# Kernel optimization log

Hardware: AMD Instinct MI355X
Metric: run time of the kernel (lower is better)

The kernel has to match this reference:

```python
import jax, jax.numpy as jnp
import numpy as np

B, T, V, D, H, O = 64, 256, 50000, 512, 1024, 64


def setup_inputs() -> dict:
    key = jax.random.key(0)
    ks = jax.random.split(key, 8)
    s = 1.0 / np.sqrt(H)  # PyTorch GRU/Linear init range
    x = jax.random.randint(ks[0], (B, T), 0, V)
    emb = jax.random.normal(ks[1], (V, D), dtype=jnp.float32) * 0.02
    W_ih = jax.random.uniform(ks[2], (3 * H, D), jnp.float32, -s, s)
    W_hh = jax.random.uniform(ks[3], (3 * H, H), jnp.float32, -s, s)
    b_ih = jax.random.uniform(ks[4], (3 * H,), jnp.float32, -s, s)
    b_hh = jax.random.uniform(ks[5], (3 * H,), jnp.float32, -s, s)
    W_fc = jax.random.uniform(ks[6], (O, H), jnp.float32, -s, s)
    b_fc = jax.random.uniform(ks[7], (O,), jnp.float32, -s, s)
    return {"x": x, "emb": emb, "W_ih": W_ih, "W_hh": W_hh,
            "b_ih": b_ih, "b_hh": b_hh, "W_fc": W_fc, "b_fc": b_fc}


def _gru_seq(gates_x, W_hh, b_hh, h0):
    # gates_x: [T, B, 3H] precomputed input contributions (r|z|n order, as PyTorch)
    def step(h, gx):
        gh = h @ W_hh.T + b_hh                       # [B, 3H]
        xr, xz, xn = jnp.split(gx, 3, axis=-1)
        hr, hz, hn = jnpp_split(gh) if False else jnp.split(gh, 3, axis=-1)
        r = jax.nn.sigmoid(xr + hr)
        z = jax.nn.sigmoid(xz + hz)
        n = jnp.tanh(xn + r * hn)
        h_new = (1.0 - z) * n + z * h
        return h_new, h_new

    _, hs = jax.lax.scan(step, h0, gates_x)          # hs: [T, B, H]
    return hs


def reference(x, emb, W_ih, W_hh, b_ih, b_hh, W_fc, b_fc):
    xe = emb[x]                                      # [B, T, D]
    # Precompute all input-to-gate projections in one GEMM: [B, T, 3H]
    gates_x = jnp.einsum('btd,gd->btg', xe, W_ih) + b_ih
    h0 = jnp.zeros((x.shape[0], W_hh.shape[1]), dtype=xe.dtype)
    hs = _gru_seq(jnp.swapaxes(gates_x, 0, 1), W_hh, b_hh, h0)  # [T, B, H]
    out = jnp.swapaxes(hs, 0, 1)                     # [B, T, H]
    logits = jnp.einsum('bth,oh->bto', out, W_fc) + b_fc
    proba = jax.nn.sigmoid(logits)
    predicted_labels = (proba > 0.5).astype(jnp.float32)
    return proba, predicted_labels
```

## Files before the change

### kernel.cpp

```cpp
#include <hip/hip_runtime.h>
#include <math.h>

#define B_   64
#define T_   256
#define D_   512
#define H_   1024
#define G3_  3072
#define O_   64
#define NTOK (B_*T_)
#define TC_  64
#define NCH_ 4

__global__ __launch_bounds__(256) void init_ws(double* __restrict__ hs,
                                               int* __restrict__ flags)
{
  int idx = blockIdx.x*256 + threadIdx.x;
  hs[idx] = 0.0;
  if (idx < 4096) flags[idx] = 0;
}

__global__ __launch_bounds__(256) void stage_a(
    const int* __restrict__ x, const float* __restrict__ emb,
    const float* __restrict__ W_ih, const float* __restrict__ b_ih,
    double* __restrict__ gx, int t_base)
{
  __shared__ float As[64][33];
  __shared__ float Bs[64][33];
  const int tid = threadIdx.x;
  const int b = blockIdx.x & 63, nBlk = blockIdx.x >> 6;
  const int g0 = nBlk*64;

  const int r = tid >> 2, c8 = tid & 3;
  const float* ap = emb  + (size_t)x[b*T_ + t_base + r]*D_ + c8*8;
  const float* bp = W_ih + (size_t)(g0 + r)*D_ + c8*8;
  const int tx = tid & 15, ty = tid >> 4;

  double acc[4][4];
  #pragma unroll
  for (int i = 0; i < 4; ++i)
    #pragma unroll
    for (int j = 0; j < 4; ++j) acc[i][j] = 0.0;

  float4 a0 = *(const float4*)(ap), a1 = *(const float4*)(ap + 4);
  float4 b0 = *(const float4*)(bp), b1 = *(const float4*)(bp + 4);

  for (int kb = 0; kb < 16; ++kb){
    __syncthreads();
    As[r][c8*8+0]=a0.x; As[r][c8*8+1]=a0.y; As[r][c8*8+2]=a0.z; As[r][c8*8+3]=a0.w;
    As[r][c8*8+4]=a1.x; As[r][c8*8+5]=a1.y; As[r][c8*8+6]=a1.z; As[r][c8*8+7]=a1.w;
    Bs[r][c8*8+0]=b0.x; Bs[r][c8*8+1]=b0.y; Bs[r][c8*8+2]=b0.z; Bs[r][c8*8+3]=b0.w;
    Bs[r][c8*8+4]=b1.x; Bs[r][c8*8+5]=b1.y; Bs[r][c8*8+6]=b1.z; Bs[r][c8*8+7]=b1.w;
    __syncthreads();
    if (kb < 15){
      a0 = *(const float4*)(ap + (kb+1)*32);  a1 = *(const float4*)(ap + (kb+1)*32 + 4);
      b0 = *(const float4*)(bp + (kb+1)*32);  b1 = *(const float4*)(bp + (kb+1)*32 + 4);
    }
    #pragma unroll
    for (int k = 0; k < 32; ++k){
      double av[4], bv[4];
      #pragma unroll
      for (int i = 0; i < 4; ++i) av[i] = (double)As[ty*4+i][k];
      #pragma unroll
      for (int j = 0; j < 4; ++j) bv[j] = (double)Bs[tx*4+j][k];
      #pragma unroll
      for (int i = 0; i < 4; ++i)
        #pragma unroll
        for (int j = 0; j < 4; ++j) acc[i][j] = fma(av[i], bv[j], acc[i][j]);
    }
  }

  double bi[4];
  #pragma unroll
  for (int j = 0; j < 4; ++j) bi[j] = (double)b_ih[g0 + tx*4 + j];
  #pragma unroll
  for (int i = 0; i < 4; ++i){
    int tl = ty*4 + i;
    size_t rowoff = ((size_t)tl*B_ + b)*G3_ + g0 + tx*4;
    #pragma unroll
    for (int j = 0; j < 4; ++j)
      gx[rowoff + j] = acc[i][j] + bi[j];
  }
}

__global__ __launch_bounds__(256, 1) void gru_rec(
    const float* __restrict__ W_hh, const float* __restrict__ b_hh,
    const double* __restrict__ gx, double* __restrict__ hs,
    int* __restrict__ flags, int t_base)
{
  __shared__ double Wl[2*12*514];
  __shared__ int abort_flag;
  const int tid = threadIdx.x, wg = blockIdx.x;
  const int i0 = wg*4;
  if (tid == 0) abort_flag = 0;

  for (int it = tid; it < 12*1024; it += 256){
    int rr = it >> 10, k = it & 1023;
    int p = rr >> 2, j = rr & 3;
    int hf = k >> 9, kl = k & 511;
    Wl[(hf*12 + rr)*514 + kl] = (double)W_hh[(size_t)(p*H_ + i0 + j)*H_ + k];
  }

  const int bq = tid >> 3, j = (tid >> 1) & 3, half = tid & 1;
  const int b_out = bq*2 + half;
  const int jj = i0 + j;
  const double bh0 = (double)b_hh[jj];
  const double bh1 = (double)b_hh[H_   + jj];
  const double bh2 = (double)b_hh[2*H_ + jj];
  const double2* w0p = (const double2*)&Wl[(half*12 + 0*4 + j)*514];
  const double2* w1p = (const double2*)&Wl[(half*12 + 1*4 + j)*514];
  const double2* w2p = (const double2*)&Wl[(half*12 + 2*4 + j)*514];
  __syncthreads();

  double hprev = hs[(size_t)b_out*H_ + jj];

  for (int tt = 0; tt < TC_; ++tt){
    const int t = t_base + tt;

    const double* gp = gx + ((size_t)tt*B_ + b_out)*G3_ + jj;
    double gxr = gp[0];
    double gxz = gp[H_];
    double gxn = gp[2*H_];

    {
      int* fp = flags + tid*16;
      int gcnt = 0;
      while (__hip_atomic_load(fp, __ATOMIC_RELAXED, __HIP_MEMORY_SCOPE_AGENT) < t){
        __builtin_amdgcn_s_sleep(2);
        if (++gcnt > (1<<18)) { abort_flag = 1; break; }
      }
    }
    __syncthreads();
    if (abort_flag) break;

    const double2* h0 = (const double2*)(hs + ((size_t)tt*B_ + bq*2    )*H_ + half*512);
    const double2* h1 = (const double2*)(hs + ((size_t)tt*B_ + bq*2 + 1)*H_ + half*512);

    double pr00=0.0, pr10=0.0, pr20=0.0, pr01=0.0, pr11=0.0, pr21=0.0;
    #pragma unroll 8
    for (int kk = 0; kk < 256; ++kk){
      double2 a0 = h0[kk];
      double2 a1 = h1[kk];
      double2 w0 = w0p[kk];
      double2 w1 = w1p[kk];
      double2 w2 = w2p[kk];
      pr00 = fma(a0.x, w0.x, pr00); pr00 = fma(a0.y, w0.y, pr00);
      pr10 = fma(a0.x, w1.x, pr10); pr10 = fma(a0.y, w1.y, pr10);
      pr20 = fma(a0.x, w2.x, pr20); pr20 = fma(a0.y, w2.y, pr20);
      pr01 = fma(a1.x, w0.x, pr01); pr01 = fma(a1.y, w0.y, pr01);
      pr11 = fma(a1.x, w1.x, pr11); pr11 = fma(a1.y, w1.y, pr11);
      pr21 = fma(a1.x, w2.x, pr21); pr21 = fma(a1.y, w2.y, pr21);
    }
    double s00 = pr00 + __shfl_xor(pr00, 1);
    double s01 = pr01 + __shfl_xor(pr01, 1);
    double s10 = pr10 + __shfl_xor(pr10, 1);
    double s11 = pr11 + __shfl_xor(pr11, 1);
    double s20 = pr20 + __shfl_xor(pr20, 1);
    double s21 = pr21 + __shfl_xor(pr21, 1);
    double ar = half ? s01 : s00;
    double az = half ? s11 : s10;
    double an = half ? s21 : s20;

    double rr_ = 1.0/(1.0 + exp(-(gxr + ar + bh0)));
    double zz  = 1.0/(1.0 + exp(-(gxz + az + bh1)));
    double nn  = tanh(gxn + rr_*(an + bh2));
    double hnew = (1.0 - zz)*nn + zz*hprev;
    hprev = hnew;

    __hip_atomic_store(&hs[((size_t)(tt+1)*B_ + b_out)*H_ + jj], hnew,
                       __ATOMIC_RELAXED, __HIP_MEMORY_SCOPE_AGENT);
    if (tt == TC_-1)
      __hip_atomic_store(&hs[(size_t)b_out*H_ + jj], hnew,
                         __ATOMIC_RELAXED, __HIP_MEMORY_SCOPE_AGENT);

    asm volatile("s_waitcnt vmcnt(0)" ::: "memory");
    __syncthreads();
    if (tid == 0)
      __hip_atomic_store(flags + wg*16, t+1, __ATOMIC_RELAXED, __HIP_MEMORY_SCOPE_AGENT);
  }
}

__global__ __launch_bounds__(256) void fc_out(
    const double* __restrict__ hs, const float* __restrict__ W_fc,
    const float* __restrict__ b_fc, float* __restrict__ out, int t_base)
{
  __shared__ double Ah[64][34];
  __shared__ double Bw[64][34];
  const int tid = threadIdx.x;
  const int b = blockIdx.x;
  const int r = tid >> 2, c8 = tid & 3;
  const double* ap = hs   + ((size_t)(r+1)*B_ + b)*H_ + c8*8;
  const float*  bp = W_fc + (size_t)r*H_ + c8*8;
  const int tx = tid & 15, ty = tid >> 4;

  double acc[4][4];
  #pragma unroll
  for (int i = 0; i < 4; ++i)
    #pragma unroll
    for (int j = 0; j < 4; ++j) acc[i][j] = 0.0;

  double ar0[8]; float br0[8];
  #pragma unroll
  for (int e = 0; e < 8; ++e){ ar0[e] = ap[e]; br0[e] = bp[e]; }

  for (int kb = 0; kb < 32; ++kb){
    __syncthreads();
    #pragma unroll
    for (int e = 0; e < 8; ++e){
      Ah[r][c8*8+e] = ar0[e];
      Bw[r][c8*8+e] = (double)br0[e];
    }
    __syncthreads();
    if (kb < 31){
      #pragma unroll
      for (int e = 0; e < 8; ++e){
        ar0[e] = ap[(kb+1)*32 + e];
        br0[e] = bp[(kb+1)*32 + e];
      }
    }
    #pragma unroll
    for (int k = 0; k < 32; ++k){
      double av[4], bv[4];
      #pragma unroll
      for (int i = 0; i < 4; ++i) av[i] = Ah[ty*4+i][k];
      #pragma unroll
      for (int j = 0; j < 4; ++j) bv[j] = Bw[tx*4+j][k];
      #pragma unroll
      for (int i = 0; i < 4; ++i)
        #pragma unroll
        for (int j = 0; j < 4; ++j) acc[i][j] = fma(av[i], bv[j], acc[i][j]);
    }
  }

  double bi[4];
  #pragma unroll
  for (int j = 0; j < 4; ++j) bi[j] = (double)b_fc[tx*4 + j];
  #pragma unroll
  for (int i = 0; i < 4; ++i){
    int tl = ty*4 + i;
    size_t tok = (size_t)b*T_ + t_base + tl;
    float4 pr, lb;
    float* prp = (float*)&pr; float* lbp = (float*)&lb;
    #pragma unroll
    for (int j = 0; j < 4; ++j){
      double logit = acc[i][j] + bi[j];
      prp[j] = (float)(1.0/(1.0 + exp(-logit)));
      float lf = (float)logit;
      float ef = (float)exp(-(double)lf);
      float pf = 1.0f / (1.0f + ef);
      lbp[j] = (pf > 0.5f) ? 1.0f : 0.0f;
    }
    *(float4*)&out[tok*O_ + tx*4] = pr;
    *(float4*)&out[(size_t)NTOK*O_ + tok*O_ + tx*4] = lb;
  }
}

extern "C" void kernel_launch(void* const* d_in, const int* in_sizes, int n_in,
                              void* d_out, int out_size, void* d_ws, size_t ws_size,
                              hipStream_t stream) {
  const int*   x    = (const int*)  d_in[0];
  const float* emb  = (const float*)d_in[1];
  const float* W_ih = (const float*)d_in[2];
  const float* W_hh = (const float*)d_in[3];
  const float* b_ih = (const float*)d_in[4];
  const float* b_hh = (const float*)d_in[5];
  const float* W_fc = (const float*)d_in[6];
  const float* b_fc = (const float*)d_in[7];
  float* out = (float*)d_out;
  char* ws = (char*)d_ws;

  double* gx    = (double*)(ws);
  double* hs    = (double*)(ws + 100663296);
  int*    flags = (int*)   (ws + 134742016);

  hipLaunchKernelGGL(init_ws, dim3(256), dim3(256), 0, stream, hs, flags);
  for (int c = 0; c < NCH_; ++c){
    int t_base = c*TC_;
    hipLaunchKernelGGL(stage_a, dim3(3072), dim3(256), 0, stream,
                       x, emb, W_ih, b_ih, gx, t_base);
    hipLaunchKernelGGL(gru_rec, dim3(256), dim3(256), 0, stream,
                       W_hh, b_hh, gx, hs, flags, t_base);
    hipLaunchKernelGGL(fc_out, dim3(64), dim3(256), 0, stream,
                       hs, W_fc, b_fc, out, t_base);
  }
}
```

Measured before the change: 9.848 ms.

## Split GRU recurrence K-dimension across 8 lanes with 512-thread blocks

The persistent GRU recurrence kernel now runs 512 threads per block. Each thread handles a 128-wide slice of the hidden dimension for 4 batch rows, instead of a 512-wide slice for 2 rows, and partial sums are combined with a three-level butterfly shuffle. This shortens the serial dot-product chain per timestep and gives each loaded weight more reuse across batch rows. The cost is redundant loads of gate inputs, more shuffles and more register pressure, and only half the threads store results.

New measurement: 17.12 ms. +73.8%, slower.

```diff
diff --git a/kernel.cpp b/kernel.cpp
--- a/kernel.cpp
+++ b/kernel.cpp
@@ -82,33 +82,37 @@
   }
 }
 
-__global__ __launch_bounds__(256, 1) void gru_rec(
+__global__ __launch_bounds__(512, 1) void gru_rec(
     const float* __restrict__ W_hh, const float* __restrict__ b_hh,
     const double* __restrict__ gx, double* __restrict__ hs,
     int* __restrict__ flags, int t_base)
 {
-  __shared__ double Wl[2*12*514];
+  __shared__ double Wl[96*130];
   __shared__ int abort_flag;
   const int tid = threadIdx.x, wg = blockIdx.x;
   const int i0 = wg*4;
   if (tid == 0) abort_flag = 0;
 
-  for (int it = tid; it < 12*1024; it += 256){
-    int rr = it >> 10, k = it & 1023;
+  for (int idx = tid; idx < 12*1024; idx += 512){
+    int rr = idx >> 10, k = idx & 1023;
     int p = rr >> 2, j = rr & 3;
-    int hf = k >> 9, kl = k & 511;
-    Wl[(hf*12 + rr)*514 + kl] = (double)W_hh[(size_t)(p*H_ + i0 + j)*H_ + k];
-  }
-
-  const int bq = tid >> 3, j = (tid >> 1) & 3, half = tid & 1;
-  const int b_out = bq*2 + half;
+    int ksl = k >> 7, kl = k & 127;
+    Wl[(rr*8 + ksl)*130 + kl] = (double)W_hh[(size_t)(p*H_ + i0 + j)*H_ + k];
+  }
+
+  const int ks = tid & 7;
+  const int j  = (tid >> 3) & 3;
+  const int bg = tid >> 5;
+  const int b0 = bg*4;
+  const int b_out = b0 + (ks & 3);
+  const bool owner = (ks < 4);
   const int jj = i0 + j;
   const double bh0 = (double)b_hh[jj];
   const double bh1 = (double)b_hh[H_   + jj];
   const double bh2 = (double)b_hh[2*H_ + jj];
-  const double2* w0p = (const double2*)&Wl[(half*12 + 0*4 + j)*514];
-  const double2* w1p = (const double2*)&Wl[(half*12 + 1*4 + j)*514];
-  const double2* w2p = (const double2*)&Wl[(half*12 + 2*4 + j)*514];
+  const double2* w0p = (const double2*)&Wl[((0*4 + j)*8 + ks)*130];
+  const double2* w1p = (const double2*)&Wl[((1*4 + j)*8 + ks)*130];
+  const double2* w2p = (const double2*)&Wl[((2*4 + j)*8 + ks)*130];
   __syncthreads();
 
   double hprev = hs[(size_t)b_out*H_ + jj];
@@ -121,7 +125,7 @@
     double gxz = gp[H_];
     double gxn = gp[2*H_];
 
-    {
+    if (tid < 256){
       int* fp = flags + tid*16;
       int gcnt = 0;
       while (__hip_atomic_load(fp, __ATOMIC_RELAXED, __HIP_MEMORY_SCOPE_AGENT) < t){
@@ -132,45 +136,64 @@
     __syncthreads();
     if (abort_flag) break;
 
-    const double2* h0 = (const double2*)(hs + ((size_t)tt*B_ + bq*2    )*H_ + half*512);
-    const double2* h1 = (const double2*)(hs + ((size_t)tt*B_ + bq*2 + 1)*H_ + half*512);
-
-    double pr00=0.0, pr10=0.0, pr20=0.0, pr01=0.0, pr11=0.0, pr21=0.0;
-    #pragma unroll 8
-    for (int kk = 0; kk < 256; ++kk){
-      double2 a0 = h0[kk];
-      double2 a1 = h1[kk];
+    const double2* h0p = (const double2*)(hs + ((size_t)tt*B_ + b0+0)*H_ + ks*128);
+    const double2* h1p = (const double2*)(hs + ((size_t)tt*B_ + b0+1)*H_ + ks*128);
+    const double2* h2p = (const double2*)(hs + ((size_t)tt*B_ + b0+2)*H_ + ks*128);
+    const double2* h3p = (const double2*)(hs + ((size_t)tt*B_ + b0+3)*H_ + ks*128);
+
+    double pr[3][4];
+    #pragma unroll
+    for (int g = 0; g < 3; ++g)
+      #pragma unroll
+      for (int i = 0; i < 4; ++i) pr[g][i] = 0.0;
+
+    #pragma unroll 4
+    for (int kk = 0; kk < 64; ++kk){
+      double2 a[4];
+      a[0] = h0p[kk]; a[1] = h1p[kk]; a[2] = h2p[kk]; a[3] = h3p[kk];
       double2 w0 = w0p[kk];
       double2 w1 = w1p[kk];
       double2 w2 = w2p[kk];
-      pr00 = fma(a0.x, w0.x, pr00); pr00 = fma(a0.y, w0.y, pr00);
-      pr10 = fma(a0.x, w1.x, pr10); pr10 = fma(a0.y, w1.y, pr10);
-      pr20 = fma(a0.x, w2.x, pr20); pr20 = fma(a0.y, w2.y, pr20);
-      pr01 = fma(a1.x, w0.x, pr01); pr01 = fma(a1.y, w0.y, pr01);
-      pr11 = fma(a1.x, w1.x, pr11); pr11 = fma(a1.y, w1.y, pr11);
-      pr21 = fma(a1.x, w2.x, pr21); pr21 = fma(a1.y, w2.y, pr21);
-    }
-    double s00 = pr00 + __shfl_xor(pr00, 1);
-    double s01 = pr01 + __shfl_xor(pr01, 1);
-    double s10 = pr10 + __shfl_xor(pr10, 1);
-    double s11 = pr11 + __shfl_xor(pr11, 1);
-    double s20 = pr20 + __shfl_xor(pr20, 1);
-    double s21 = pr21 + __shfl_xor(pr21, 1);
-    double ar = half ? s01 : s00;
-    double az = half ? s11 : s10;
-    double an = half ? s21 : s20;
-
-    double rr_ = 1.0/(1.0 + exp(-(gxr + ar + bh0)));
-    double zz  = 1.0/(1.0 + exp(-(gxz + az + bh1)));
-    double nn  = tanh(gxn + rr_*(an + bh2));
+      #pragma unroll
+      for (int i = 0; i < 4; ++i){
+        pr[0][i] = fma(a[i].x, w0.x, pr[0][i]); pr[0][i] = fma(a[i].y, w0.y, pr[0][i]);
+        pr[1][i] = fma(a[i].x, w1.x, pr[1][i]); pr[1][i] = fma(a[i].y, w1.y, pr[1][i]);
+        pr[2][i] = fma(a[i].x, w2.x, pr[2][i]); pr[2][i] = fma(a[i].y, w2.y, pr[2][i]);
+      }
+    }
+
+    #pragma unroll
+    for (int g = 0; g < 3; ++g)
+      #pragma unroll
+      for (int i = 0; i < 4; ++i){
+        double v = pr[g][i];
+        v += __shfl_xor(v, 1);
+        v += __shfl_xor(v, 2);
+        v += __shfl_xor(v, 4);
+        pr[g][i] = v;
+      }
+
+    double sg[3];
+    #pragma unroll
+    for (int g = 0; g < 3; ++g){
+      double sA = (ks & 1) ? pr[g][1] : pr[g][0];
+      double sB = (ks & 1) ? pr[g][3] : pr[g][2];
+      sg[g] = (ks & 2) ? sB : sA;
+    }
+
+    double rr_ = 1.0/(1.0 + exp(-(gxr + sg[0] + bh0)));
+    double zz  = 1.0/(1.0 + exp(-(gxz + sg[1] + bh1)));
+    double nn  = tanh(gxn + rr_*(sg[2] + bh2));
     double hnew = (1.0 - zz)*nn + zz*hprev;
     hprev = hnew;
 
-    __hip_atomic_store(&hs[((size_t)(tt+1)*B_ + b_out)*H_ + jj], hnew,
-                       __ATOMIC_RELAXED, __HIP_MEMORY_SCOPE_AGENT);
-    if (tt == TC_-1)
-      __hip_atomic_store(&hs[(size_t)b_out*H_ + jj], hnew,
+    if (owner){
+      __hip_atomic_store(&hs[((size_t)(tt+1)*B_ + b_out)*H_ + jj], hnew,
                          __ATOMIC_RELAXED, __HIP_MEMORY_SCOPE_AGENT);
+      if (tt == TC_-1)
+        __hip_atomic_store(&hs[(size_t)b_out*H_ + jj], hnew,
+                           __ATOMIC_RELAXED, __HIP_MEMORY_SCOPE_AGENT);
+    }
 
     asm volatile("s_waitcnt vmcnt(0)" ::: "memory");
     __syncthreads();
@@ -277,7 +300,7 @@
     int t_base = c*TC_;
     hipLaunchKernelGGL(stage_a, dim3(3072), dim3(256), 0, stream,
                        x, emb, W_ih, b_ih, gx, t_base);
-    hipLaunchKernelGGL(gru_rec, dim3(256), dim3(256), 0, stream,
+    hipLaunchKernelGGL(gru_rec, dim3(256), dim3(512), 0, stream,
                        W_hh, b_hh, gx, hs, flags, t_base);
     hipLaunchKernelGGL(fc_out, dim3(64), dim3(256), 0, stream,
                        hs, W_fc, b_fc, out, t_base);
```

## Register-tile GRU recurrence over 4 batches x 4 columns with shuffle-tree reduction

Applied to the files above, without the earlier changes.

Replaces the LDS-staged fp64 copy of the W_hh slice with float4 reads straight from global memory (which should stay in cache across timesteps). Each thread now computes a 4-batch by 4-column by 3-gate register tile over a 64-element slice of k, instead of 2 batches by 3 gates over half of k. The 16 k-partials are combined with a butterfly of xor shuffles that halves the live values at each level. This raises reuse of h and W per load and drops the LDS weight traffic. In exchange it carries 48 fp64 accumulators per thread (register pressure) and depends on cache hits for the weights every step.

Result: slower. 15.45 ms (+56.9%).

```diff
diff --git a/kernel.cpp b/kernel.cpp
--- a/kernel.cpp
+++ b/kernel.cpp
@@ -87,36 +87,36 @@
     const double* __restrict__ gx, double* __restrict__ hs,
     int* __restrict__ flags, int t_base)
 {
-  __shared__ double Wl[2*12*514];
   __shared__ int abort_flag;
   const int tid = threadIdx.x, wg = blockIdx.x;
   const int i0 = wg*4;
   if (tid == 0) abort_flag = 0;
 
-  for (int it = tid; it < 12*1024; it += 256){
-    int rr = it >> 10, k = it & 1023;
-    int p = rr >> 2, j = rr & 3;
-    int hf = k >> 9, kl = k & 511;
-    Wl[(hf*12 + rr)*514 + kl] = (double)W_hh[(size_t)(p*H_ + i0 + j)*H_ + k];
-  }
-
-  const int bq = tid >> 3, j = (tid >> 1) & 3, half = tid & 1;
-  const int b_out = bq*2 + half;
-  const int jj = i0 + j;
-  const double bh0 = (double)b_hh[jj];
-  const double bh1 = (double)b_hh[H_   + jj];
-  const double bh2 = (double)b_hh[2*H_ + jj];
-  const double2* w0p = (const double2*)&Wl[(half*12 + 0*4 + j)*514];
-  const double2* w1p = (const double2*)&Wl[(half*12 + 1*4 + j)*514];
-  const double2* w2p = (const double2*)&Wl[(half*12 + 2*4 + j)*514];
+  const int bq4 = tid >> 4, k16 = tid & 15;
+  const int B0  = bq4*4;
+  const int cb1 = (k16 >> 3) & 1, cb0 = (k16 >> 2) & 1;
+  const int bb1 = (k16 >> 1) & 1, bb0 = k16 & 1;
+  const int b_out = B0 + (k16 & 3);
+  const int c_out = i0 + (k16 >> 2);
+
+  const double bh0 = (double)b_hh[c_out];
+  const double bh1 = (double)b_hh[H_   + c_out];
+  const double bh2 = (double)b_hh[2*H_ + c_out];
+
+  const float4* wp[3][4];
+  #pragma unroll
+  for (int p = 0; p < 3; ++p)
+    #pragma unroll
+    for (int c = 0; c < 4; ++c)
+      wp[p][c] = (const float4*)(W_hh + (size_t)(p*H_ + i0 + c)*H_ + k16*64);
+
+  double hprev = hs[(size_t)b_out*H_ + c_out];
   __syncthreads();
-
-  double hprev = hs[(size_t)b_out*H_ + jj];
 
   for (int tt = 0; tt < TC_; ++tt){
     const int t = t_base + tt;
 
-    const double* gp = gx + ((size_t)tt*B_ + b_out)*G3_ + jj;
+    const double* gp = gx + ((size_t)tt*B_ + b_out)*G3_ + c_out;
     double gxr = gp[0];
     double gxz = gp[H_];
     double gxn = gp[2*H_];
@@ -132,44 +132,111 @@
     __syncthreads();
     if (abort_flag) break;
 
-    const double2* h0 = (const double2*)(hs + ((size_t)tt*B_ + bq*2    )*H_ + half*512);
-    const double2* h1 = (const double2*)(hs + ((size_t)tt*B_ + bq*2 + 1)*H_ + half*512);
-
-    double pr00=0.0, pr10=0.0, pr20=0.0, pr01=0.0, pr11=0.0, pr21=0.0;
-    #pragma unroll 8
-    for (int kk = 0; kk < 256; ++kk){
-      double2 a0 = h0[kk];
-      double2 a1 = h1[kk];
-      double2 w0 = w0p[kk];
-      double2 w1 = w1p[kk];
-      double2 w2 = w2p[kk];
-      pr00 = fma(a0.x, w0.x, pr00); pr00 = fma(a0.y, w0.y, pr00);
-      pr10 = fma(a0.x, w1.x, pr10); pr10 = fma(a0.y, w1.y, pr10);
-      pr20 = fma(a0.x, w2.x, pr20); pr20 = fma(a0.y, w2.y, pr20);
-      pr01 = fma(a1.x, w0.x, pr01); pr01 = fma(a1.y, w0.y, pr01);
-      pr11 = fma(a1.x, w1.x, pr11); pr11 = fma(a1.y, w1.y, pr11);
-      pr21 = fma(a1.x, w2.x, pr21); pr21 = fma(a1.y, w2.y, pr21);
-    }
-    double s00 = pr00 + __shfl_xor(pr00, 1);
-    double s01 = pr01 + __shfl_xor(pr01, 1);
-    double s10 = pr10 + __shfl_xor(pr10, 1);
-    double s11 = pr11 + __shfl_xor(pr11, 1);
-    double s20 = pr20 + __shfl_xor(pr20, 1);
-    double s21 = pr21 + __shfl_xor(pr21, 1);
-    double ar = half ? s01 : s00;
-    double az = half ? s11 : s10;
-    double an = half ? s21 : s20;
-
-    double rr_ = 1.0/(1.0 + exp(-(gxr + ar + bh0)));
-    double zz  = 1.0/(1.0 + exp(-(gxz + az + bh1)));
-    double nn  = tanh(gxn + rr_*(an + bh2));
+    const double2* hp[4];
+    #pragma unroll
+    for (int bi = 0; bi < 4; ++bi)
+      hp[bi] = (const double2*)(hs + ((size_t)tt*B_ + B0 + bi)*H_ + k16*64);
+
+    double P[4][4][3];
+    #pragma unroll
+    for (int bi = 0; bi < 4; ++bi)
+      #pragma unroll
+      for (int c = 0; c < 4; ++c)
+        #pragma unroll
+        for (int p = 0; p < 3; ++p) P[bi][c][p] = 0.0;
+
+    #pragma unroll 2
+    for (int g4 = 0; g4 < 16; ++g4){
+      double2 h0[4], h1[4];
+      #pragma unroll
+      for (int bi = 0; bi < 4; ++bi){
+        h0[bi] = hp[bi][2*g4];
+        h1[bi] = hp[bi][2*g4+1];
+      }
+      float4 wv[3][4];
+      #pragma unroll
+      for (int p = 0; p < 3; ++p)
+        #pragma unroll
+        for (int c = 0; c < 4; ++c) wv[p][c] = wp[p][c][g4];
+
+      #pragma unroll
+      for (int p = 0; p < 3; ++p)
+        #pragma unroll
+        for (int c = 0; c < 4; ++c){
+          double w0 = (double)wv[p][c].x;
+          double w1 = (double)wv[p][c].y;
+          double w2 = (double)wv[p][c].z;
+          double w3 = (double)wv[p][c].w;
+          #pragma unroll
+          for (int bi = 0; bi < 4; ++bi){
+            double a = P[bi][c][p];
+            a = fma(h0[bi].x, w0, a);
+            a = fma(h0[bi].y, w1, a);
+            a = fma(h1[bi].x, w2, a);
+            a = fma(h1[bi].y, w3, a);
+            P[bi][c][p] = a;
+          }
+        }
+    }
+
+    #pragma unroll
+    for (int bi = 0; bi < 4; ++bi)
+      #pragma unroll
+      for (int c = 0; c < 4; ++c)
+        #pragma unroll
+        for (int p = 0; p < 3; ++p)
+          P[bi][c][p] += __shfl_xor(P[bi][c][p], 8);
+    double L24[4][2][3];
+    #pragma unroll
+    for (int bi = 0; bi < 4; ++bi)
+      #pragma unroll
+      for (int dc = 0; dc < 2; ++dc)
+        #pragma unroll
+        for (int p = 0; p < 3; ++p)
+          L24[bi][dc][p] = cb1 ? P[bi][2+dc][p] : P[bi][dc][p];
+    #pragma unroll
+    for (int bi = 0; bi < 4; ++bi)
+      #pragma unroll
+      for (int dc = 0; dc < 2; ++dc)
+        #pragma unroll
+        for (int p = 0; p < 3; ++p)
+          L24[bi][dc][p] += __shfl_xor(L24[bi][dc][p], 4);
+    double L12[4][3];
+    #pragma unroll
+    for (int bi = 0; bi < 4; ++bi)
+      #pragma unroll
+      for (int p = 0; p < 3; ++p)
+        L12[bi][p] = cb0 ? L24[bi][1][p] : L24[bi][0][p];
+    #pragma unroll
+    for (int bi = 0; bi < 4; ++bi)
+      #pragma unroll
+      for (int p = 0; p < 3; ++p)
+        L12[bi][p] += __shfl_xor(L12[bi][p], 2);
+    double L6[2][3];
+    #pragma unroll
+    for (int db = 0; db < 2; ++db)
+      #pragma unroll
+      for (int p = 0; p < 3; ++p)
+        L6[db][p] = bb1 ? L12[2+db][p] : L12[db][p];
+    #pragma unroll
+    for (int db = 0; db < 2; ++db)
+      #pragma unroll
+      for (int p = 0; p < 3; ++p)
+        L6[db][p] += __shfl_xor(L6[db][p], 1);
+    double sg0 = bb0 ? L6[1][0] : L6[0][0];
+    double sg1 = bb0 ? L6[1][1] : L6[0][1];
+    double sg2 = bb0 ? L6[1][2] : L6[0][2];
+
+    double rr_ = 1.0/(1.0 + exp(-(gxr + sg0 + bh0)));
+    double zz  = 1.0/(1.0 + exp(-(gxz + sg1 + bh1)));
+    double nn  = tanh(gxn + rr_*(sg2 + bh2));
     double hnew = (1.0 - zz)*nn + zz*hprev;
     hprev = hnew;
 
-    __hip_atomic_store(&hs[((size_t)(tt+1)*B_ + b_out)*H_ + jj], hnew,
+    __hip_atomic_store(&hs[((size_t)(tt+1)*B_ + b_out)*H_ + c_out], hnew,
                        __ATOMIC_RELAXED, __HIP_MEMORY_SCOPE_AGENT);
     if (tt == TC_-1)
-      __hip_atomic_store(&hs[(size_t)b_out*H_ + jj], hnew,
+      __hip_atomic_store(&hs[(size_t)b_out*H_ + c_out], hnew,
                          __ATOMIC_RELAXED, __HIP_MEMORY_SCOPE_AGENT);
 
     asm volatile("s_waitcnt vmcnt(0)" ::: "memory");
```
